# Performance work log

Measured on AMD Instinct MI355X. Metric: run time of the kernel, lower is better.

Reference implementation:

```python
import jax, jax.numpy as jnp
import numpy as np

D_MODEL = 1024
NUM_HEADS = 16
HEAD_DIM = 64
INNER = NUM_HEADS * HEAD_DIM


def setup_inputs() -> dict:
    key = jax.random.key(0)
    k_x, k_q, k_k, k_v, k_o = jax.random.split(key, 5)
    B, T = 4, 2048
    s = 1.0 / np.sqrt(D_MODEL)
    return {
        "x": jax.random.normal(k_x, (B, T, D_MODEL), dtype=jnp.float32),
        "W_q": jax.random.uniform(k_q, (D_MODEL, INNER), dtype=jnp.float32, minval=-s, maxval=s),
        "W_k": jax.random.uniform(k_k, (D_MODEL, INNER), dtype=jnp.float32, minval=-s, maxval=s),
        "W_v": jax.random.uniform(k_v, (D_MODEL, INNER), dtype=jnp.float32, minval=-s, maxval=s),
        "W_o": jax.random.uniform(k_o, (INNER, D_MODEL), dtype=jnp.float32, minval=-s, maxval=s),
    }


def reference(x, W_q, W_k, W_v, W_o):
    B, T, _ = x.shape
    scale = HEAD_DIM ** -0.5
    # project and split heads: [B, H, T, Dh]
    q = (x @ W_q).reshape(B, T, NUM_HEADS, HEAD_DIM).transpose(0, 2, 1, 3)
    k = (x @ W_k).reshape(B, T, NUM_HEADS, HEAD_DIM).transpose(0, 2, 1, 3)
    v = (x @ W_v).reshape(B, T, NUM_HEADS, HEAD_DIM).transpose(0, 2, 1, 3)
    scores = jnp.einsum("bhqd,bhkd->bhqk", q, k) * scale  # [B,H,T,T]
    causal = jnp.tril(jnp.ones((T, T), dtype=bool))
    scores = jnp.where(causal, scores, -jnp.inf)
    probs = jax.nn.softmax(scores, axis=-1)
    ctx = jnp.einsum("bhqk,bhkd->bhqd", probs, v)
    ctx = ctx.transpose(0, 2, 1, 3).reshape(B, T, INNER)
    return ctx @ W_o
```

## Files before the change

### kernel.cpp

```cpp
#include <hip/hip_runtime.h>


typedef short  short8  __attribute__((ext_vector_type(8)));
typedef short  short4v __attribute__((ext_vector_type(4)));
typedef float  floatx4 __attribute__((ext_vector_type(4)));
typedef unsigned uint2v __attribute__((ext_vector_type(2)));

#define T_SZ 2048
#define DM   1024

#define QSCALE 0.18033688011112042f

__device__ __forceinline__ short f2bf(float f) {
  unsigned u = __float_as_uint(f);
  u += 0x7fffu + ((u >> 16) & 1u);
  return (short)(u >> 16);
}

#if defined(__has_builtin) && __has_builtin(__builtin_amdgcn_cvt_pk_bf16_f32)
typedef __bf16 bf16x2_t __attribute__((ext_vector_type(2)));
__device__ __forceinline__ unsigned pack_bf(float lo, float hi) {
  return __builtin_bit_cast(unsigned, __builtin_amdgcn_cvt_pk_bf16_f32(lo, hi));
}
#else
__device__ __forceinline__ unsigned pack_bf(float lo, float hi) {
  return __builtin_amdgcn_perm(__float_as_uint(hi) + 0x8000u,
                               __float_as_uint(lo) + 0x8000u, 0x07060302u);
}
#endif

#if defined(__has_builtin) && __has_builtin(__builtin_amdgcn_exp2f)
__device__ __forceinline__ float fexp2(float x) { return __builtin_amdgcn_exp2f(x); }
#else
__device__ __forceinline__ float fexp2(float x) { return exp2f(x); }
#endif

__device__ __forceinline__ void gll16(const void* g, void* l) {
  __builtin_amdgcn_global_load_lds((const __attribute__((address_space(1))) void*)g,
                                   (__attribute__((address_space(3))) void*)l, 16, 0, 0);
}

__global__ void cvt_kernel(const float* __restrict__ s0, const float* __restrict__ s1,
                           const float* __restrict__ s2, const float* __restrict__ s3,
                           short* __restrict__ dst,
                           const float* __restrict__ x, short* __restrict__ xb) {
  const int tx = threadIdx.x, ty = threadIdx.y;
  if (blockIdx.z == 4) {
    const int tid = ty * 32 + tx;
    const int blk = blockIdx.y * 32 + blockIdx.x;
    int i = (blk * 256 + tid) * 4;
#pragma unroll
    for (int j = 0; j < 8; ++j) {
      const float4 v = *(const float4*)(x + i);
      short4v o;
      o.x = f2bf(v.x); o.y = f2bf(v.y); o.z = f2bf(v.z); o.w = f2bf(v.w);
      *(short4v*)(xb + i) = o;
      i += 1048576;
    }
    return;
  }
  const float* srcs[4] = {s0, s1, s2, s3};
  const float* src = srcs[blockIdx.z];
  short* d = dst + (size_t)blockIdx.z * 1048576;
  __shared__ float tile[32][33];
  const int n_base = blockIdx.x * 32, k_base = blockIdx.y * 32;
#pragma unroll
  for (int j = 0; j < 4; ++j)
    tile[ty + j * 8][tx] = src[(size_t)(k_base + ty + j * 8) * 1024 + n_base + tx];
  __syncthreads();
#pragma unroll
  for (int j = 0; j < 4; ++j)
    d[(size_t)(n_base + ty + j * 8) * 1024 + k_base + tx] = f2bf(tile[tx][ty + j * 8]);
}

template <int MODE>
__global__ void gemm_bt(const short* __restrict__ A, const short* __restrict__ Bt,
                        short* __restrict__ obf, short* __restrict__ vt,
                        float* __restrict__ of, int K) {
  __shared__ short As[128 * 32];
  __shared__ short Bs[128 * 32];
  const int tid  = threadIdx.x;
  const int w    = tid >> 6, lane = tid & 63;
  const int quad = lane >> 4, l15 = lane & 15;
  const int wr   = w >> 1, wc = w & 1;
  const int lid  = (int)blockIdx.y * 64 + (int)blockIdx.x;
  const int m0   = (((lid & 7) + 8 * ((lid >> 3) & 7))) * 128;
  const int n0   = (lid >> 6) * 128;
  const int arow = tid >> 2, apart = tid & 3;

  floatx4 acc[4][4] = {};

  for (int kk = 0; kk < K; kk += 32) {
    gll16(A  + (size_t)(m0 + arow) * K      + kk + apart * 8, &As[tid * 8]);
    gll16(A  + (size_t)(m0 + 64 + arow) * K + kk + apart * 8, &As[(256 + tid) * 8]);
    gll16(Bt + (size_t)(n0 + arow) * K      + kk + apart * 8, &Bs[tid * 8]);
    gll16(Bt + (size_t)(n0 + 64 + arow) * K + kk + apart * 8, &Bs[(256 + tid) * 8]);
    __syncthreads();
    short8 af[4], bf[4];
#pragma unroll
    for (int i = 0; i < 4; ++i)
      af[i] = *(const short8*)&As[(wr * 64 + i * 16 + l15) * 32 + quad * 8];
#pragma unroll
    for (int j = 0; j < 4; ++j)
      bf[j] = *(const short8*)&Bs[(wc * 64 + j * 16 + l15) * 32 + quad * 8];
#pragma unroll
    for (int i = 0; i < 4; ++i)
#pragma unroll
      for (int j = 0; j < 4; ++j)
        acc[i][j] = __builtin_amdgcn_mfma_f32_16x16x32_bf16(af[i], bf[j], acc[i][j], 0, 0, 0);
    __syncthreads();
  }

  if (MODE == 0) {
    const int wsel = n0 >> 10;
    const int ncol0 = (n0 & 1023) + wc * 64;
    if (wsel < 2) {
      const float scale = (wsel == 0) ? QSCALE : 1.0f;
      short* outw = obf + (size_t)wsel * (64u * 2048u * 64u);
#pragma unroll
      for (int i = 0; i < 4; ++i) {
        const int row0 = m0 + wr * 64 + i * 16 + quad * 4;
#pragma unroll
        for (int j = 0; j < 4; ++j) {
          const int col = ncol0 + j * 16 + l15;
          const int h = col >> 6, d = col & 63;
#pragma unroll
          for (int r = 0; r < 4; ++r) {
            const int rg = row0 + r;
            const int b = rg >> 11, t = rg & 2047;
            outw[(((size_t)(b * 16 + h) * 2048 + t) << 6) + d] = f2bf(acc[i][j][r] * scale);
          }
        }
      }
    } else {
#pragma unroll
      for (int i = 0; i < 4; ++i) {
        const int row0 = m0 + wr * 64 + i * 16 + quad * 4;
        const int b = row0 >> 11, t = row0 & 2047;
#pragma unroll
        for (int j = 0; j < 4; ++j) {
          const int col = ncol0 + j * 16 + l15;
          const int h = col >> 6, d = col & 63;
          short4v pv;
#pragma unroll
          for (int r = 0; r < 4; ++r) pv[r] = f2bf(acc[i][j][r]);
          *(short4v*)(vt + (((size_t)(b * 16 + h) * 64 + d) << 11) + t) = pv;
        }
      }
    }
  } else {
#pragma unroll
    for (int i = 0; i < 4; ++i) {
      const int row0 = m0 + wr * 64 + i * 16 + quad * 4;
#pragma unroll
      for (int j = 0; j < 4; ++j) {
        const int col = n0 + wc * 64 + j * 16 + l15;
#pragma unroll
        for (int r = 0; r < 4; ++r)
          of[(size_t)(row0 + r) * 1024 + col] = acc[i][j][r];
      }
    }
  }
}

__global__ __launch_bounds__(256, 2) void attn_kernel(
    const short* __restrict__ Qg, const short* __restrict__ Kg,
    const short* __restrict__ Vt, short* __restrict__ ctx) {
  __shared__ short Ks[128 * 72];
  __shared__ short Vs[80 * 132];
  __shared__ short Ps[4 * 32 * 136];

  const int tid  = threadIdx.x;
  const int w    = tid >> 6, lane = tid & 63;
  const int quad = lane >> 4, l15 = lane & 15;
  const int bh = (int)blockIdx.x + 8 * ((int)blockIdx.y & 7);
  const int p  = (int)blockIdx.y >> 3;
  const int b  = bh >> 4, h = bh & 15;

  const size_t base = (size_t)bh * (T_SZ * 64);
  const short* Qb  = Qg + base;
  const short* Kb  = Kg + base;
  const short* Vtb = Vt + base;
  short* Pw = &Ps[w * (32 * 136)];

  const int skr = tid >> 1, skc = (tid & 1) * 32;
  const int svr = tid >> 2, svc = (tid & 3) * 32;

  {
    const int rr = 64 + (tid >> 4), cb = (tid & 15) * 8;
    const short vv = (tid < 16) ? (short)0x3F80 : (short)0;
    short8 fill;
#pragma unroll
    for (int j = 0; j < 8; ++j) fill[j] = vv;
    *(short8*)&Vs[rr * 132 + cb] = fill;
  }

  for (int qsel = 0; qsel < 2; ++qsel) {
    const int qi = qsel ? (15 - p) : p;
    const int q0 = qi << 7;
    const int rowA = q0 + w * 32;
    const int rowB = rowA + 16;

    const short8 qA0 = *(const short8*)(Qb + (size_t)(rowA + l15) * 64 + quad * 8);
    const short8 qA1 = *(const short8*)(Qb + (size_t)(rowA + l15) * 64 + 32 + quad * 8);
    const short8 qB0 = *(const short8*)(Qb + (size_t)(rowB + l15) * 64 + quad * 8);
    const short8 qB1 = *(const short8*)(Qb + (size_t)(rowB + l15) * 64 + 32 + quad * 8);

    floatx4 OA[4] = {}, OB[4] = {};
    floatx4 O5A = {}, O5B = {};

    const int ktiles = qi + 1;
    short8 kR[4], vR[4];
#pragma unroll
    for (int j = 0; j < 4; ++j) {
      kR[j] = *(const short8*)(Kb + (size_t)skr * 64 + skc + j * 8);
      vR[j] = *(const short8*)(Vtb + (size_t)svr * 2048 + svc + j * 8);
    }

    for (int kt = 0; kt < ktiles; ++kt) {
      const int k0 = kt << 7;
      __syncthreads();
#pragma unroll
      for (int j = 0; j < 4; ++j) {
        *(short8*)&Ks[skr * 72 + skc + j * 8] = kR[j];
        *(short8*)&Vs[svr * 132 + svc + j * 8] = vR[j];
      }
      if (kt + 1 < ktiles) {
        const int kn = (kt + 1) << 7;
#pragma unroll
        for (int j = 0; j < 4; ++j) {
          kR[j] = *(const short8*)(Kb + (size_t)(kn + skr) * 64 + skc + j * 8);
          vR[j] = *(const short8*)(Vtb + (size_t)svr * 2048 + kn + svc + j * 8);
        }
      }
      __syncthreads();

      const int dkA = rowA - k0;
      const int dkB = dkA + 16;
      const int limA = dkA + l15, limB = limA + 16;
      const int naA = min(8, (dkA >> 4) + 1), nchA = (naA + 1) >> 1;
      const int naB = min(8, (dkB >> 4) + 1), nchB = (naB + 1) >> 1;

#pragma unroll
      for (int mt = 0; mt < 8; ++mt) {
        const int pa = l15 * 136 + mt * 16 + quad * 4;
        const int pb = (16 + l15) * 136 + mt * 16 + quad * 4;
        const bool actA = (mt * 16 < dkA + 16);
        const bool actB = (mt * 16 < dkB + 16);
        if (actB) {
          const short8 kf0 = *(const short8*)&Ks[(mt * 16 + l15) * 72 + quad * 8];
          const short8 kf1 = *(const short8*)&Ks[(mt * 16 + l15) * 72 + 32 + quad * 8];
          {
            floatx4 s = {};
            s = __builtin_amdgcn_mfma_f32_16x16x32_bf16(kf0, qB0, s, 0, 0, 0);
            s = __builtin_amdgcn_mfma_f32_16x16x32_bf16(kf1, qB1, s, 0, 0, 0);
            if (mt * 16 + 15 > dkB) {
#pragma unroll
              for (int r = 0; r < 4; ++r)
                if (mt * 16 + quad * 4 + r > limB) s[r] = -1e30f;
            }
            floatx4 e;
#pragma unroll
            for (int r = 0; r < 4; ++r) e[r] = fexp2(s[r]);
            uint2v pd;
            pd.x = pack_bf(e[0], e[1]);
            pd.y = pack_bf(e[2], e[3]);
            *(uint2v*)&Pw[pb] = pd;
          }
          if (actA) {
            floatx4 s = {};
            s = __builtin_amdgcn_mfma_f32_16x16x32_bf16(kf0, qA0, s, 0, 0, 0);
            s = __builtin_amdgcn_mfma_f32_16x16x32_bf16(kf1, qA1, s, 0, 0, 0);
            if (mt * 16 + 15 > dkA) {
#pragma unroll
              for (int r = 0; r < 4; ++r)
                if (mt * 16 + quad * 4 + r > limA) s[r] = -1e30f;
            }
            floatx4 e;
#pragma unroll
            for (int r = 0; r < 4; ++r) e[r] = fexp2(s[r]);
            uint2v pd;
            pd.x = pack_bf(e[0], e[1]);
            pd.y = pack_bf(e[2], e[3]);
            *(uint2v*)&Pw[pa] = pd;
          } else if (mt < 2 * nchA) {
            uint2v z; z.x = 0; z.y = 0;
            *(uint2v*)&Pw[pa] = z;
          }
        } else {
          uint2v z; z.x = 0; z.y = 0;
          if (mt < 2 * nchB) *(uint2v*)&Pw[pb] = z;
          if (mt < 2 * nchA) *(uint2v*)&Pw[pa] = z;
        }
      }

#pragma unroll
      for (int c = 0; c < 4; ++c) {
        if (c < nchB) {
          const short8 vfl = *(const short8*)&Vs[(64 + l15) * 132 + c * 32 + quad * 8];
          short8 vf[4];
#pragma unroll
          for (int dt = 0; dt < 4; ++dt)
            vf[dt] = *(const short8*)&Vs[(dt * 16 + l15) * 132 + c * 32 + quad * 8];
          const short8 pfB = *(const short8*)&Pw[(16 + l15) * 136 + c * 32 + quad * 8];
#pragma unroll
          for (int dt = 0; dt < 4; ++dt)
            OB[dt] = __builtin_amdgcn_mfma_f32_16x16x32_bf16(vf[dt], pfB, OB[dt], 0, 0, 0);
          O5B = __builtin_amdgcn_mfma_f32_16x16x32_bf16(vfl, pfB, O5B, 0, 0, 0);
          if (c < nchA) {
            const short8 pfA = *(const short8*)&Pw[l15 * 136 + c * 32 + quad * 8];
#pragma unroll
            for (int dt = 0; dt < 4; ++dt)
              OA[dt] = __builtin_amdgcn_mfma_f32_16x16x32_bf16(vf[dt], pfA, OA[dt], 0, 0, 0);
            O5A = __builtin_amdgcn_mfma_f32_16x16x32_bf16(vfl, pfA, O5A, 0, 0, 0);
          }
        }
      }
    }

    {
      const float lA = __shfl(O5A[0], l15);
      const float invA = 1.0f / lA;
      const int t = rowA + l15;
      short* cb = ctx + (((size_t)(b * T_SZ + t)) << 10) + h * 64 + quad * 4;
#pragma unroll
      for (int dt = 0; dt < 4; ++dt) {
        short4v o4;
#pragma unroll
        for (int r = 0; r < 4; ++r) o4[r] = f2bf(OA[dt][r] * invA);
        *(short4v*)(cb + dt * 16) = o4;
      }
    }
    {
      const float lB = __shfl(O5B[0], l15);
      const float invB = 1.0f / lB;
      const int t = rowB + l15;
      short* cb = ctx + (((size_t)(b * T_SZ + t)) << 10) + h * 64 + quad * 4;
#pragma unroll
      for (int dt = 0; dt < 4; ++dt) {
        short4v o4;
#pragma unroll
        for (int r = 0; r < 4; ++r) o4[r] = f2bf(OB[dt][r] * invB);
        *(short4v*)(cb + dt * 16) = o4;
      }
    }
  }
}

extern "C" void kernel_launch(void* const* d_in, const int* in_sizes, int n_in,
                              void* d_out, int out_size, void* d_ws, size_t ws_size,
                              hipStream_t stream) {
  const float* x  = (const float*)d_in[0];
  const float* Wq = (const float*)d_in[1];
  const float* Wk = (const float*)d_in[2];
  const float* Wv = (const float*)d_in[3];
  const float* Wo = (const float*)d_in[4];
  float* out = (float*)d_out;

  short* ws  = (short*)d_ws;
  short* xb  = ws;
  short* Wt  = ws + 8388608;
  short* Qb  = Wt + 4 * 1048576;
  short* Kb  = Qb + 8388608;
  short* Vt  = Kb + 8388608;
  short* ctx = xb;

  cvt_kernel<<<dim3(32, 32, 5), dim3(32, 8), 0, stream>>>(Wq, Wk, Wv, Wo, Wt, x, xb);
  gemm_bt<0><<<dim3(64, 24), 256, 0, stream>>>(xb, Wt, Qb, Vt, nullptr, 1024);
  attn_kernel<<<dim3(8, 64), 256, 0, stream>>>(Qb, Kb, Vt, ctx);
  gemm_bt<1><<<dim3(64, 8), 256, 0, stream>>>(ctx, Wt + 3 * 1048576, nullptr, nullptr, out, 1024);
}
```

Measured before the change: 257.8 us.

## Process paired causal query tiles together in one 512-thread attention block

The attention kernel now uses 8 waves per block. Each wave takes 16 rows from query tile p and 16 rows from its mirror tile 15-p, and one pass over the key tiles serves both, where before the two tiles were handled one after the other. Shared K/V loads are therefore reused across both query tiles and the second pass over keys disappears. The probability scratch is halved per wave by splitting the key tile into two 64-wide halves. The grid index mapping is also changed. Larger blocks raise register and LDS pressure per CU, which may reduce occupancy.

```diff
diff --git a/kernel.cpp b/kernel.cpp
--- a/kernel.cpp
+++ b/kernel.cpp
@@ -163,91 +163,84 @@
   }
 }
 
-__global__ __launch_bounds__(256, 2) void attn_kernel(
+__global__ __launch_bounds__(512, 4) void attn_kernel(
     const short* __restrict__ Qg, const short* __restrict__ Kg,
     const short* __restrict__ Vt, short* __restrict__ ctx) {
   __shared__ short Ks[128 * 72];
   __shared__ short Vs[80 * 132];
-  __shared__ short Ps[4 * 32 * 136];
+  __shared__ short Ps[8 * 32 * 68];
 
   const int tid  = threadIdx.x;
   const int w    = tid >> 6, lane = tid & 63;
   const int quad = lane >> 4, l15 = lane & 15;
   const int bh = (int)blockIdx.x + 8 * ((int)blockIdx.y & 7);
-  const int p  = (int)blockIdx.y >> 3;
+  const int g  = (int)blockIdx.y >> 3;
+  const int p  = (g < 4) ? g : 11 - g;
   const int b  = bh >> 4, h = bh & 15;
 
   const size_t base = (size_t)bh * (T_SZ * 64);
   const short* Qb  = Qg + base;
   const short* Kb  = Kg + base;
   const short* Vtb = Vt + base;
-  short* Pw = &Ps[w * (32 * 136)];
-
-  const int skr = tid >> 1, skc = (tid & 1) * 32;
-  const int svr = tid >> 2, svc = (tid & 3) * 32;
-
-  {
-    const int rr = 64 + (tid >> 4), cb = (tid & 15) * 8;
-    const short vv = (tid < 16) ? (short)0x3F80 : (short)0;
-    short8 fill;
-#pragma unroll
-    for (int j = 0; j < 8; ++j) fill[j] = vv;
-    *(short8*)&Vs[rr * 132 + cb] = fill;
-  }
-
-  for (int qsel = 0; qsel < 2; ++qsel) {
-    const int qi = qsel ? (15 - p) : p;
-    const int q0 = qi << 7;
-    const int rowA = q0 + w * 32;
-    const int rowB = rowA + 16;
-
-    const short8 qA0 = *(const short8*)(Qb + (size_t)(rowA + l15) * 64 + quad * 8);
-    const short8 qA1 = *(const short8*)(Qb + (size_t)(rowA + l15) * 64 + 32 + quad * 8);
-    const short8 qB0 = *(const short8*)(Qb + (size_t)(rowB + l15) * 64 + quad * 8);
-    const short8 qB1 = *(const short8*)(Qb + (size_t)(rowB + l15) * 64 + 32 + quad * 8);
-
-    floatx4 OA[4] = {}, OB[4] = {};
-    floatx4 O5A = {}, O5B = {};
-
-    const int ktiles = qi + 1;
-    short8 kR[4], vR[4];
-#pragma unroll
-    for (int j = 0; j < 4; ++j) {
-      kR[j] = *(const short8*)(Kb + (size_t)skr * 64 + skc + j * 8);
-      vR[j] = *(const short8*)(Vtb + (size_t)svr * 2048 + svc + j * 8);
-    }
-
-    for (int kt = 0; kt < ktiles; ++kt) {
-      const int k0 = kt << 7;
-      __syncthreads();
-#pragma unroll
-      for (int j = 0; j < 4; ++j) {
-        *(short8*)&Ks[skr * 72 + skc + j * 8] = kR[j];
-        *(short8*)&Vs[svr * 132 + svc + j * 8] = vR[j];
-      }
-      if (kt + 1 < ktiles) {
-        const int kn = (kt + 1) << 7;
-#pragma unroll
-        for (int j = 0; j < 4; ++j) {
-          kR[j] = *(const short8*)(Kb + (size_t)(kn + skr) * 64 + skc + j * 8);
-          vR[j] = *(const short8*)(Vtb + (size_t)svr * 2048 + kn + svc + j * 8);
-        }
-      }
-      __syncthreads();
-
-      const int dkA = rowA - k0;
-      const int dkB = dkA + 16;
-      const int limA = dkA + l15, limB = limA + 16;
-      const int naA = min(8, (dkA >> 4) + 1), nchA = (naA + 1) >> 1;
-      const int naB = min(8, (dkB >> 4) + 1), nchB = (naB + 1) >> 1;
-
-#pragma unroll
-      for (int mt = 0; mt < 8; ++mt) {
-        const int pa = l15 * 136 + mt * 16 + quad * 4;
-        const int pb = (16 + l15) * 136 + mt * 16 + quad * 4;
-        const bool actA = (mt * 16 < dkA + 16);
-        const bool actB = (mt * 16 < dkB + 16);
-        if (actB) {
+  short* Pw = &Ps[w * (32 * 68)];
+
+  const int skr = tid >> 2, skc = (tid & 3) * 16;
+  const int svr = tid >> 3, svc = (tid & 7) * 16;
+
+  if (tid < 17) {
+    short8 one;
+#pragma unroll
+    for (int j = 0; j < 8; ++j) one[j] = (short)0x3F80;
+    *(short8*)&Vs[64 * 132 + tid * 8] = one;
+  }
+
+  const int rowA = (p << 7) + w * 16;
+  const int rowB = ((15 - p) << 7) + w * 16;
+
+  const short8 qA0 = *(const short8*)(Qb + (size_t)(rowA + l15) * 64 + quad * 8);
+  const short8 qA1 = *(const short8*)(Qb + (size_t)(rowA + l15) * 64 + 32 + quad * 8);
+  const short8 qB0 = *(const short8*)(Qb + (size_t)(rowB + l15) * 64 + quad * 8);
+  const short8 qB1 = *(const short8*)(Qb + (size_t)(rowB + l15) * 64 + 32 + quad * 8);
+
+  floatx4 OA[4] = {}, OB[4] = {};
+  floatx4 O5A = {}, O5B = {};
+
+  const int kmax = 16 - p;
+  short8 kR0 = *(const short8*)(Kb + (size_t)skr * 64 + skc);
+  short8 kR1 = *(const short8*)(Kb + (size_t)skr * 64 + skc + 8);
+  short8 vR0 = *(const short8*)(Vtb + (size_t)svr * 2048 + svc);
+  short8 vR1 = *(const short8*)(Vtb + (size_t)svr * 2048 + svc + 8);
+
+  for (int kt = 0; kt < kmax; ++kt) {
+    const int k0 = kt << 7;
+    __syncthreads();
+    *(short8*)&Ks[skr * 72 + skc] = kR0;
+    *(short8*)&Ks[skr * 72 + skc + 8] = kR1;
+    *(short8*)&Vs[svr * 132 + svc] = vR0;
+    *(short8*)&Vs[svr * 132 + svc + 8] = vR1;
+    if (kt + 1 < kmax) {
+      const int kn = (kt + 1) << 7;
+      kR0 = *(const short8*)(Kb + (size_t)(kn + skr) * 64 + skc);
+      kR1 = *(const short8*)(Kb + (size_t)(kn + skr) * 64 + skc + 8);
+      vR0 = *(const short8*)(Vtb + (size_t)svr * 2048 + kn + svc);
+      vR1 = *(const short8*)(Vtb + (size_t)svr * 2048 + kn + svc + 8);
+    }
+    __syncthreads();
+
+    const bool aA = (kt <= p);
+    const int dkA = rowA - k0;
+    const int dkB = rowB - k0;
+    const int limA = dkA + l15, limB = dkB + l15;
+
+#pragma unroll
+    for (int half = 0; half < 2; ++half) {
+      if (half * 64 > dkB) break;
+#pragma unroll
+      for (int mt2 = 0; mt2 < 4; ++mt2) {
+        const int mt = half * 4 + mt2;
+        const int pa = l15 * 68 + mt2 * 16 + quad * 4;
+        const int pb = (16 + l15) * 68 + mt2 * 16 + quad * 4;
+        if (mt * 16 <= dkB) {
           const short8 kf0 = *(const short8*)&Ks[(mt * 16 + l15) * 72 + quad * 8];
           const short8 kf1 = *(const short8*)&Ks[(mt * 16 + l15) * 72 + 32 + quad * 8];
           {
@@ -267,7 +260,7 @@
             pd.y = pack_bf(e[2], e[3]);
             *(uint2v*)&Pw[pb] = pd;
           }
-          if (actA) {
+          if (aA && mt * 16 <= dkA) {
             floatx4 s = {};
             s = __builtin_amdgcn_mfma_f32_16x16x32_bf16(kf0, qA0, s, 0, 0, 0);
             s = __builtin_amdgcn_mfma_f32_16x16x32_bf16(kf1, qA1, s, 0, 0, 0);
@@ -283,32 +276,32 @@
             pd.x = pack_bf(e[0], e[1]);
             pd.y = pack_bf(e[2], e[3]);
             *(uint2v*)&Pw[pa] = pd;
-          } else if (mt < 2 * nchA) {
+          } else if (aA && (mt >> 1) * 32 <= dkA) {
             uint2v z; z.x = 0; z.y = 0;
             *(uint2v*)&Pw[pa] = z;
           }
         } else {
           uint2v z; z.x = 0; z.y = 0;
-          if (mt < 2 * nchB) *(uint2v*)&Pw[pb] = z;
-          if (mt < 2 * nchA) *(uint2v*)&Pw[pa] = z;
+          if ((mt >> 1) * 32 <= dkB) *(uint2v*)&Pw[pb] = z;
+          if (aA && (mt >> 1) * 32 <= dkA) *(uint2v*)&Pw[pa] = z;
         }
       }
-
-#pragma unroll
-      for (int c = 0; c < 4; ++c) {
-        if (c < nchB) {
+#pragma unroll
+      for (int cc = 0; cc < 2; ++cc) {
+        const int c = half * 2 + cc;
+        if (c * 32 <= dkB) {
           const short8 vfl = *(const short8*)&Vs[(64 + l15) * 132 + c * 32 + quad * 8];
           short8 vf[4];
 #pragma unroll
           for (int dt = 0; dt < 4; ++dt)
             vf[dt] = *(const short8*)&Vs[(dt * 16 + l15) * 132 + c * 32 + quad * 8];
-          const short8 pfB = *(const short8*)&Pw[(16 + l15) * 136 + c * 32 + quad * 8];
+          const short8 pfB = *(const short8*)&Pw[(16 + l15) * 68 + cc * 32 + quad * 8];
 #pragma unroll
           for (int dt = 0; dt < 4; ++dt)
             OB[dt] = __builtin_amdgcn_mfma_f32_16x16x32_bf16(vf[dt], pfB, OB[dt], 0, 0, 0);
           O5B = __builtin_amdgcn_mfma_f32_16x16x32_bf16(vfl, pfB, O5B, 0, 0, 0);
-          if (c < nchA) {
-            const short8 pfA = *(const short8*)&Pw[l15 * 136 + c * 32 + quad * 8];
+          if (aA && c * 32 <= dkA) {
+            const short8 pfA = *(const short8*)&Pw[l15 * 68 + cc * 32 + quad * 8];
 #pragma unroll
             for (int dt = 0; dt < 4; ++dt)
               OA[dt] = __builtin_amdgcn_mfma_f32_16x16x32_bf16(vf[dt], pfA, OA[dt], 0, 0, 0);
@@ -317,32 +310,30 @@
         }
       }
     }
-
-    {
-      const float lA = __shfl(O5A[0], l15);
-      const float invA = 1.0f / lA;
-      const int t = rowA + l15;
-      short* cb = ctx + (((size_t)(b * T_SZ + t)) << 10) + h * 64 + quad * 4;
-#pragma unroll
-      for (int dt = 0; dt < 4; ++dt) {
-        short4v o4;
-#pragma unroll
-        for (int r = 0; r < 4; ++r) o4[r] = f2bf(OA[dt][r] * invA);
-        *(short4v*)(cb + dt * 16) = o4;
-      }
-    }
-    {
-      const float lB = __shfl(O5B[0], l15);
-      const float invB = 1.0f / lB;
-      const int t = rowB + l15;
-      short* cb = ctx + (((size_t)(b * T_SZ + t)) << 10) + h * 64 + quad * 4;
-#pragma unroll
-      for (int dt = 0; dt < 4; ++dt) {
-        short4v o4;
-#pragma unroll
-        for (int r = 0; r < 4; ++r) o4[r] = f2bf(OB[dt][r] * invB);
-        *(short4v*)(cb + dt * 16) = o4;
-      }
+  }
+
+  {
+    const float invA = 1.0f / __shfl(O5A[0], l15);
+    const int t = rowA + l15;
+    short* cb = ctx + (((size_t)(b * T_SZ + t)) << 10) + h * 64 + quad * 4;
+#pragma unroll
+    for (int dt = 0; dt < 4; ++dt) {
+      short4v o4;
+#pragma unroll
+      for (int r = 0; r < 4; ++r) o4[r] = f2bf(OA[dt][r] * invA);
+      *(short4v*)(cb + dt * 16) = o4;
+    }
+  }
+  {
+    const float invB = 1.0f / __shfl(O5B[0], l15);
+    const int t = rowB + l15;
+    short* cb = ctx + (((size_t)(b * T_SZ + t)) << 10) + h * 64 + quad * 4;
+#pragma unroll
+    for (int dt = 0; dt < 4; ++dt) {
+      short4v o4;
+#pragma unroll
+      for (int r = 0; r < 4; ++r) o4[r] = f2bf(OB[dt][r] * invB);
+      *(short4v*)(cb + dt * 16) = o4;
     }
   }
 }
@@ -367,6 +358,6 @@
 
   cvt_kernel<<<dim3(32, 32, 5), dim3(32, 8), 0, stream>>>(Wq, Wk, Wv, Wo, Wt, x, xb);
   gemm_bt<0><<<dim3(64, 24), 256, 0, stream>>>(xb, Wt, Qb, Vt, nullptr, 1024);
-  attn_kernel<<<dim3(8, 64), 256, 0, stream>>>(Qb, Kb, Vt, ctx);
+  attn_kernel<<<dim3(8, 64), 512, 0, stream>>>(Qb, Kb, Vt, ctx);
   gemm_bt<1><<<dim3(64, 8), 256, 0, stream>>>(ctx, Wt + 3 * 1048576, nullptr, nullptr, out, 1024);
 }
```

New measurement: 263.9 us. 1.02x slower.
